# Kernel optimization log

Measured on AMD Instinct MI355X. Metric: run time of the kernel, lower is better.

## Reference

```python
import jax, jax.numpy as jnp
import numpy as np

DIM = 1024
H = 16
DQK = 64   # head_qk_dim = dim*expand_k / num_heads
DV = 64    # head_v_dim
DIN = 4    # dim_inner (fast-weight rows)
CHUNK = 16
BASE_LR = 1e-3
KS = 4     # short conv kernel size
LN_EPS = 1e-5


def short_conv(x, w):
    """Causal depthwise conv1d (kernel KS) + identity residual.
    x: [b, l, c], w: [c, KS] (tap j multiplies x[t - (KS-1) + j])."""
    b, l, c = x.shape
    xp = jnp.pad(x, ((0, 0), (KS - 1, 0), (0, 0)))
    y = x  # residual: y = conv(x) + x
    for j in range(KS):
        y = y + xp[:, j:j + l, :] * w[None, None, :, j]
    return y


def setup_inputs() -> dict:
    key = jax.random.key(0)
    ks = jax.random.split(key, 16)
    b, l = 4, 2048
    key_dim, value_dim = H * DQK, H * DV
    inp = {
        "hidden_states": jax.random.normal(ks[0], (b, l, DIM), jnp.float32),
        "Wq": jax.random.normal(ks[1], (key_dim, DIM), jnp.float32) / np.sqrt(DIM),
        "Wk": jax.random.normal(ks[2], (key_dim, DIM), jnp.float32) / np.sqrt(DIM),
        "Wv": jax.random.normal(ks[3], (value_dim, DIM), jnp.float32) / np.sqrt(DIM),
        "Wlr": jax.random.normal(ks[4], (2 * H, DIM), jnp.float32) / np.sqrt(DIM),
        "Wo": jax.random.normal(ks[5], (DIM, value_dim), jnp.float32) / np.sqrt(value_dim),
        "Wg": jax.random.normal(ks[6], (DIM, value_dim), jnp.float32) / np.sqrt(value_dim),
        "conv_q": jax.random.normal(ks[7], (key_dim, KS), jnp.float32) / np.sqrt(KS),
        "conv_k": jax.random.normal(ks[8], (key_dim, KS), jnp.float32) / np.sqrt(KS),
        "conv_v": jax.random.normal(ks[9], (value_dim, KS), jnp.float32) / np.sqrt(KS),
        "W_in_init": jax.random.normal(ks[10], (1, DIN, H, DQK), jnp.float32) / np.sqrt(DQK),
        "W_out_init": jax.random.normal(ks[11], (1, DIN, H, DV), jnp.float32) / np.sqrt(DIN),
        "ln_gamma": jnp.ones((DV,), jnp.float32),
        "ln_beta": jnp.zeros((DV,), jnp.float32),
    }
    return inp


def reference(hidden_states, Wq, Wk, Wv, Wlr, Wo, Wg,
              conv_q, conv_k, conv_v, W_in_init, W_out_init, ln_gamma, ln_beta):
    b, l, _ = hidden_states.shape
    scale = 1.0 / np.sqrt(DQK)

    q = short_conv(hidden_states @ Wq.T, conv_q).reshape(b, l, H, DQK)
    k = short_conv(hidden_states @ Wk.T, conv_k).reshape(b, l, H, DQK)
    v = short_conv(hidden_states @ Wv.T, conv_v).reshape(b, l, H, DV)

    lr = jax.nn.softplus(hidden_states @ Wlr.T + BASE_LR).reshape(b, l, H, 2)

    nC = l // CHUNK
    # [nC, b, CHUNK, H, d] for scan over chunks
    qc = q.reshape(b, nC, CHUNK, H, DQK).transpose(1, 0, 2, 3, 4)
    kc = k.reshape(b, nC, CHUNK, H, DQK).transpose(1, 0, 2, 3, 4)
    vc = v.reshape(b, nC, CHUNK, H, DV).transpose(1, 0, 2, 3, 4)
    lrc = lr.reshape(b, nC, CHUNK, H, 2).transpose(1, 0, 2, 3, 4)

    W_in0 = jnp.broadcast_to(W_in_init, (b, DIN, H, DQK))
    W_out0 = jnp.broadcast_to(W_out_init, (b, DIN, H, DV))

    # causal mask: query t (abs pos DIN+t) sees keys j <= DIN+t
    mask = jnp.arange(DIN + CHUNK)[None, :] <= (jnp.arange(CHUNK)[:, None] + DIN)

    def step(carry, xs):
        W_in, W_out = carry
        qch, kch, vch, lrch = xs  # [b, CHUNK, H, d]
        Kf = jnp.concatenate([W_in, kch], axis=1)   # [b, DIN+CHUNK, H, DQK]
        Vf = jnp.concatenate([W_out, vch], axis=1)  # [b, DIN+CHUNK, H, DV]
        s = jnp.einsum('bthd,bshd->bhts', qch, Kf) * scale
        s = jnp.where(mask[None, None], s, -jnp.inf)
        o = jnp.einsum('bhts,bshd->bthd', jax.nn.softmax(s, axis=-1), Vf)

        # fast_kk update rule (non-causal attention, queries = W_in rows)
        g1 = jnp.einsum('bnhd,bchd->bhnc', W_in, kch) * scale
        Grad_out = -jnp.einsum('bhnc,bchd->bnhd', jax.nn.softmax(g1, -1), vch)
        g2 = jnp.einsum('bnhd,bchd->bhnc', W_in, kch * 0.5) * scale
        Grad_in = -jnp.einsum('bhnc,bchd->bnhd', jax.nn.softmax(g2, -1), kch)

        lr_mean = jnp.mean(lrch, axis=1, keepdims=True)  # [b,1,H,2]
        W_in_new = W_in - lr_mean[..., 0:1] * Grad_in
        W_out_new = W_out - lr_mean[..., 1:2] * Grad_out
        return (W_in_new, W_out_new), o

    _, os = jax.lax.scan(step, (W_in0, W_out0), (qc, kc, vc, lrc))
    o = os.transpose(1, 0, 2, 3, 4).reshape(b, l, H, DV)

    # LayerNorm over head_v_dim
    mu = o.mean(-1, keepdims=True)
    var = o.var(-1, keepdims=True)
    o = (o - mu) / jnp.sqrt(var + LN_EPS) * ln_gamma + ln_beta
    o = o.reshape(b, l, H * DV)

    gate = hidden_states @ Wg.T
    return (o * gate) @ Wo.T
```

## Files before the change

### kernel.cpp

```cpp
#include <hip/hip_runtime.h>
#include <hip/hip_bf16.h>
#include <math.h>

#define BATCH 4
#define SEQ   2048
#define DIM   1024
#define NH    16
#define DQK   64
#define DV    64
#define DIN   4
#define CHUNK 16
#define NC    128
#define KS    4
#define TOK   (BATCH*SEQ)
#define SCALE 0.125f
#define BASE_LR 1e-3f
#define LN_EPS 1e-5f
#define K3    3072

typedef float f32x4 __attribute__((ext_vector_type(4)));
typedef short s16x8 __attribute__((ext_vector_type(8)));

__device__ __forceinline__ unsigned short f2bf(float f) {
    unsigned u = __float_as_uint(f);
    u += 0x7fffu + ((u >> 16) & 1u);
    return (unsigned short)(u >> 16);
}
__device__ __forceinline__ float bf2f(unsigned short h) {
    return __uint_as_float(((unsigned)h) << 16);
}

__device__ __forceinline__ void gload_lds16(const void* g, void* l) {
    __builtin_amdgcn_global_load_lds(
        (const __attribute__((address_space(1))) void*)g,
        (__attribute__((address_space(3))) void*)l, 16, 0, 0);
}

__global__ __launch_bounds__(256) void split_bf16_kernel(
    const float* __restrict__ X, unsigned short* __restrict__ Y,
    int rows, int wmode)
{
    const int idx = blockIdx.x * 256 + threadIdx.x;
    if (idx >= rows * (DIM / 4)) return;
    const int r  = idx >> 8;
    const int c4 = (idx & 255) << 2;

    float4 x = *(const float4*)(X + (size_t)r * DIM + c4);
    ushort4 hv, lv;
    hv.x = f2bf(x.x); lv.x = f2bf(x.x - bf2f(hv.x));
    hv.y = f2bf(x.y); lv.y = f2bf(x.y - bf2f(hv.y));
    hv.z = f2bf(x.z); lv.z = f2bf(x.z - bf2f(hv.z));
    hv.w = f2bf(x.w); lv.w = f2bf(x.w - bf2f(hv.w));

    const size_t rb = (size_t)r * K3;
    *(ushort4*)(Y + rb + c4)        = hv;
    *(ushort4*)(Y + rb + 1024 + c4) = wmode ? lv : hv;
    *(ushort4*)(Y + rb + 2048 + c4) = wmode ? hv : lv;
}

__global__ __launch_bounds__(256) void gemm_mfma_qkvg(
    const unsigned short* __restrict__ A, const unsigned short* __restrict__ B,
    float* __restrict__ Cq, float* __restrict__ Ck,
    float* __restrict__ Cv, float* __restrict__ Cg)
{
    __shared__ __align__(16) unsigned short sA[128 * 64];
    __shared__ __align__(16) unsigned short sB[128 * 64];

    const int tid  = threadIdx.x;
    const int lane = tid & 63;
    const int wav  = tid >> 6;

    const int nbx = gridDim.x;
    const int nwg = nbx * gridDim.y;
    int flat = blockIdx.x + blockIdx.y * nbx;
    const int per = nwg >> 3;
    flat = (flat & 7) * per + (flat >> 3);
    const int m0 = (flat / nbx) * 128;
    const int n0 = (flat % nbx) * 128;

    const int wm = (wav >> 1) * 64;
    const int wn = (wav & 1) * 64;

    f32x4 acc[4][4] = {};

    const int fbase = wav * 64 + lane;
    const int lrow  = lane & 15;
    const int g     = lane >> 4;

    for (int kt = 0; kt < K3; kt += 64) {
        __syncthreads();
#pragma unroll
        for (int i = 0; i < 4; ++i) {
            const int f  = fbase + i * 256;
            const int r  = f >> 3;
            const int c  = (f & 7) ^ (r & 7);
            const size_t go = (size_t)r * K3 + kt + c * 8;
            char* lb = (char*)sA + (wav * 64 + i * 256) * 16;
            gload_lds16(A + (size_t)m0 * K3 + go, lb);
        }
#pragma unroll
        for (int i = 0; i < 4; ++i) {
            const int f  = fbase + i * 256;
            const int r  = f >> 3;
            const int c  = (f & 7) ^ (r & 7);
            const size_t go = (size_t)r * K3 + kt + c * 8;
            char* lb = (char*)sB + (wav * 64 + i * 256) * 16;
            gload_lds16(B + (size_t)n0 * K3 + go, lb);
        }
        __syncthreads();

#pragma unroll
        for (int ks = 0; ks < 2; ++ks) {
            const int cbase = ks * 4 + g;
            s16x8 af[4], bfr[4];
#pragma unroll
            for (int mi = 0; mi < 4; ++mi) {
                const int r  = wm + mi * 16 + lrow;
                const int cs = cbase ^ (r & 7);
                af[mi] = *(const s16x8*)((const char*)sA + r * 128 + cs * 16);
            }
#pragma unroll
            for (int ni = 0; ni < 4; ++ni) {
                const int r  = wn + ni * 16 + lrow;
                const int cs = cbase ^ (r & 7);
                bfr[ni] = *(const s16x8*)((const char*)sB + r * 128 + cs * 16);
            }
#pragma unroll
            for (int mi = 0; mi < 4; ++mi)
#pragma unroll
                for (int ni = 0; ni < 4; ++ni)
                    acc[mi][ni] = __builtin_amdgcn_mfma_f32_16x16x32_bf16(
                        af[mi], bfr[ni], acc[mi][ni], 0, 0, 0);
        }
    }

    const int nblk = n0 >> 10;
    float* __restrict__ Co = (nblk == 0) ? Cq : (nblk == 1) ? Ck
                           : (nblk == 2) ? Cv : Cg;
    const int nc0 = (n0 & 1023) + wn;
    const int lcol = lane & 15;
    const int lq   = lane >> 4;
#pragma unroll
    for (int mi = 0; mi < 4; ++mi)
#pragma unroll
        for (int ni = 0; ni < 4; ++ni)
#pragma unroll
            for (int r = 0; r < 4; ++r) {
                const int m = m0 + wm + mi * 16 + lq * 4 + r;
                const int n = nc0 + ni * 16 + lcol;
                Co[(size_t)m * DIM + n] = acc[mi][ni][r];
            }
}

__global__ __launch_bounds__(256) void gemm_mfma_bt(
    const unsigned short* __restrict__ A, const unsigned short* __restrict__ B,
    float* __restrict__ C, int M, int N)
{
    __shared__ __align__(16) unsigned short sA[128 * 64];
    __shared__ __align__(16) unsigned short sB[128 * 64];

    const int tid  = threadIdx.x;
    const int lane = tid & 63;
    const int wav  = tid >> 6;

    const int nbx = gridDim.x;
    const int nwg = nbx * gridDim.y;
    int flat = blockIdx.x + blockIdx.y * nbx;
    const int per = nwg >> 3;
    flat = (flat & 7) * per + (flat >> 3);
    const int m0 = (flat / nbx) * 128;
    const int n0 = (flat % nbx) * 128;

    const int wm = (wav >> 1) * 64;
    const int wn = (wav & 1) * 64;

    f32x4 acc[4][4] = {};

    const int fbase = wav * 64 + lane;
    const int lrow  = lane & 15;
    const int g     = lane >> 4;

    for (int kt = 0; kt < K3; kt += 64) {
        __syncthreads();
#pragma unroll
        for (int i = 0; i < 4; ++i) {
            const int f  = fbase + i * 256;
            const int r  = f >> 3;
            const int c  = (f & 7) ^ (r & 7);
            const size_t go = (size_t)r * K3 + kt + c * 8;
            char* lb = (char*)sA + (wav * 64 + i * 256) * 16;
            gload_lds16(A + (size_t)m0 * K3 + go, lb);
        }
#pragma unroll
        for (int i = 0; i < 4; ++i) {
            const int f  = fbase + i * 256;
            const int r  = f >> 3;
            const int c  = (f & 7) ^ (r & 7);
            const size_t go = (size_t)r * K3 + kt + c * 8;
            char* lb = (char*)sB + (wav * 64 + i * 256) * 16;
            gload_lds16(B + (size_t)n0 * K3 + go, lb);
        }
        __syncthreads();

#pragma unroll
        for (int ks = 0; ks < 2; ++ks) {
            const int cbase = ks * 4 + g;
            s16x8 af[4], bfr[4];
#pragma unroll
            for (int mi = 0; mi < 4; ++mi) {
                const int r  = wm + mi * 16 + lrow;
                const int cs = cbase ^ (r & 7);
                af[mi] = *(const s16x8*)((const char*)sA + r * 128 + cs * 16);
            }
#pragma unroll
            for (int ni = 0; ni < 4; ++ni) {
                const int r  = wn + ni * 16 + lrow;
                const int cs = cbase ^ (r & 7);
                bfr[ni] = *(const s16x8*)((const char*)sB + r * 128 + cs * 16);
            }
#pragma unroll
            for (int mi = 0; mi < 4; ++mi)
#pragma unroll
                for (int ni = 0; ni < 4; ++ni)
                    acc[mi][ni] = __builtin_amdgcn_mfma_f32_16x16x32_bf16(
                        af[mi], bfr[ni], acc[mi][ni], 0, 0, 0);
        }
    }

    const int lcol = lane & 15;
    const int lq   = lane >> 4;
#pragma unroll
    for (int mi = 0; mi < 4; ++mi)
#pragma unroll
        for (int ni = 0; ni < 4; ++ni)
#pragma unroll
            for (int r = 0; r < 4; ++r) {
                const int m = m0 + wm + mi * 16 + lq * 4 + r;
                const int n = n0 + wn + ni * 16 + lcol;
                C[(size_t)m * N + n] = acc[mi][ni][r];
            }
}

#define GBM 128
#define GBN 128
#define GBK 8

__global__ __launch_bounds__(256) void gemm_nt_f32(
    const float* __restrict__ A, const float* __restrict__ B,
    float* __restrict__ C, int M, int N, int K)
{
    __shared__ float As[GBK][GBM + 4];
    __shared__ float Bs[GBK][GBN + 4];

    const int tid = threadIdx.x;
    const int m0 = blockIdx.y * GBM;
    const int n0 = blockIdx.x * GBN;
    const int la_m = tid >> 1;
    const int la_k = (tid & 1) << 2;
    const int tm = tid >> 4;
    const int tn = tid & 15;

    float acc[8][8] = {};

    const float* Arow = A + (size_t)(m0 + la_m) * K + la_k;
    const float* Brow = B + (size_t)(n0 + la_m) * K + la_k;
    const bool bvalid = (n0 + la_m) < N;

    for (int k0 = 0; k0 < K; k0 += GBK) {
        float4 av = *(const float4*)(Arow + k0);
        float4 bv = make_float4(0.f, 0.f, 0.f, 0.f);
        if (bvalid) bv = *(const float4*)(Brow + k0);

        __syncthreads();
        As[la_k + 0][la_m] = av.x; As[la_k + 1][la_m] = av.y;
        As[la_k + 2][la_m] = av.z; As[la_k + 3][la_m] = av.w;
        Bs[la_k + 0][la_m] = bv.x; Bs[la_k + 1][la_m] = bv.y;
        Bs[la_k + 2][la_m] = bv.z; Bs[la_k + 3][la_m] = bv.w;
        __syncthreads();

#pragma unroll
        for (int k = 0; k < GBK; ++k) {
            float4 a0 = *(const float4*)&As[k][tm * 8];
            float4 a1 = *(const float4*)&As[k][tm * 8 + 4];
            float4 b0 = *(const float4*)&Bs[k][tn * 8];
            float4 b1 = *(const float4*)&Bs[k][tn * 8 + 4];
            float a[8] = {a0.x, a0.y, a0.z, a0.w, a1.x, a1.y, a1.z, a1.w};
            float b[8] = {b0.x, b0.y, b0.z, b0.w, b1.x, b1.y, b1.z, b1.w};
#pragma unroll
            for (int i = 0; i < 8; ++i)
#pragma unroll
                for (int j = 0; j < 8; ++j)
                    acc[i][j] += a[i] * b[j];
        }
    }

#pragma unroll
    for (int i = 0; i < 8; ++i) {
        const int m = m0 + tm * 8 + i;
#pragma unroll
        for (int j = 0; j < 8; ++j) {
            const int n = n0 + tn * 8 + j;
            if (n < N) C[(size_t)m * N + n] = acc[i][j];
        }
    }
}

__global__ __launch_bounds__(256) void conv_res_kernel(
    const float* __restrict__ x, const float* __restrict__ w,
    float* __restrict__ y)
{
    const int tid = blockIdx.x * blockDim.x + threadIdx.x;
    if (tid >= TOK * 256) return;
    const int c4  = (tid & 255) << 2;
    const int row = tid >> 8;
    const int t   = row & (SEQ - 1);

    const float* xp = x + (size_t)row * DIM + c4;
    float4 acc = *(const float4*)xp;
    float4 w0 = *(const float4*)(w + (c4 + 0) * 4);
    float4 w1 = *(const float4*)(w + (c4 + 1) * 4);
    float4 w2 = *(const float4*)(w + (c4 + 2) * 4);
    float4 w3 = *(const float4*)(w + (c4 + 3) * 4);

#pragma unroll
    for (int j = 0; j < 4; ++j) {
        const int tt = t - 3 + j;
        if (tt >= 0) {
            float4 xv = *(const float4*)(xp + (j - 3) * DIM);
            acc.x += xv.x * ((&w0.x)[j]);
            acc.y += xv.y * ((&w1.x)[j]);
            acc.z += xv.z * ((&w2.x)[j]);
            acc.w += xv.w * ((&w3.x)[j]);
        }
    }
    *(float4*)(y + (size_t)row * DIM + c4) = acc;
}

__global__ __launch_bounds__(256) void lrmean_kernel(
    const float* __restrict__ lrpre, float* __restrict__ lrm)
{
    const int idx = blockIdx.x * blockDim.x + threadIdx.x;
    if (idx >= BATCH * NC * NH * 2) return;
    const int j = idx & 1;
    const int h = (idx >> 1) & 15;
    const int c = (idx >> 5) & 127;
    const int b = idx >> 12;

    float s = 0.f;
#pragma unroll
    for (int i = 0; i < CHUNK; ++i) {
        float x = lrpre[((size_t)b * SEQ + c * CHUNK + i) * 32 + h * 2 + j] + BASE_LR;
        s += fmaxf(x, 0.f) + log1pf(expf(-fabsf(x)));
    }
    lrm[idx] = s * (1.f / CHUNK);
}

__global__ __launch_bounds__(128) void state_scan_kernel(
    const float* __restrict__ kconv, const float* __restrict__ vconv,
    const float* __restrict__ lrm,
    const float* __restrict__ win_init, const float* __restrict__ wout_init,
    float* __restrict__ wst_in, float* __restrict__ wst_out)
{
    const int bh  = blockIdx.x;
    const int b   = bh >> 4, h = bh & 15;
    const int tid = threadIdx.x;
    const int wv  = tid >> 6;
    const int d   = tid & 63;

    __shared__ __align__(16) float sW[DIN][68];
    __shared__ __align__(16) float sK[CHUNK][68];
    __shared__ __align__(16) float sP1[2][DIN][16];
    __shared__ __align__(16) float sP2[2][DIN][16];
    __shared__ float sLR[NC * 2];

    const float* __restrict__ xin  = wv ? vconv     : kconv;
    const float* __restrict__ wini = wv ? wout_init : win_init;
    float*       __restrict__ wst  = wv ? wst_out   : wst_in;

    float W[DIN];
#pragma unroll
    for (int n = 0; n < DIN; ++n) W[n] = wini[(n * NH + h) * 64 + d];

    sLR[tid * 2 + 0] = lrm[(((size_t)b * NC + tid) * NH + h) * 2 + 0];
    sLR[tid * 2 + 1] = lrm[(((size_t)b * NC + tid) * NH + h) * 2 + 1];

    const int gn = d >> 4;
    const int gc = d & 15;

    float xa[CHUNK], xb[CHUNK];
    const size_t base00 = (size_t)b * SEQ * DIM + h * 64 + d;
#pragma unroll
    for (int i = 0; i < CHUNK; ++i) xa[i] = xin[base00 + (size_t)i * DIM];
    asm volatile("s_waitcnt lgkmcnt(0)" ::: "memory");

#define SCAN_STEP(c, XA, XB)                                                   \
    {                                                                          \
        const int pb = (c) & 1;                                                \
        if ((c) + 1 < NC) {                                                    \
            const size_t basen = base00 + (size_t)(((c) + 1) * CHUNK) * DIM;   \
            _Pragma("unroll")                                                  \
            for (int i = 0; i < CHUNK; ++i)                                    \
                XB[i] = xin[basen + (size_t)i * DIM];                          \
        }                                                                      \
        const size_t wofs = (((size_t)bh * NC + (c)) * DIN) * 64 + d;          \
        _Pragma("unroll")                                                      \
        for (int n = 0; n < DIN; ++n) wst[wofs + n * 64] = W[n];               \
        if (wv == 0) {                                                         \
            _Pragma("unroll")                                                  \
            for (int i = 0; i < CHUNK; ++i) sK[i][d] = XA[i];                  \
            _Pragma("unroll")                                                  \
            for (int n = 0; n < DIN; ++n) sW[n][d] = W[n];                     \
            asm volatile("s_waitcnt lgkmcnt(0)" ::: "memory");                 \
            float p0 = 0.f, p1 = 0.f, p2 = 0.f, p3 = 0.f;                      \
            _Pragma("unroll")                                                  \
            for (int q = 0; q < 4; ++q) {                                      \
                const int o = q * 16;                                          \
                float4 w0 = *(const float4*)&sW[gn][o + 0];                    \
                float4 k0 = *(const float4*)&sK[gc][o + 0];                    \
                float4 w1 = *(const float4*)&sW[gn][o + 4];                    \
                float4 k1 = *(const float4*)&sK[gc][o + 4];                    \
                float4 w2 = *(const float4*)&sW[gn][o + 8];                    \
                float4 k2 = *(const float4*)&sK[gc][o + 8];                    \
                float4 w3 = *(const float4*)&sW[gn][o + 12];                   \
                float4 k3 = *(const float4*)&sK[gc][o + 12];                   \
                p0 += w0.x*k0.x; p0 += w0.y*k0.y; p0 += w0.z*k0.z; p0 += w0.w*k0.w; \
                p1 += w1.x*k1.x; p1 += w1.y*k1.y; p1 += w1.z*k1.z; p1 += w1.w*k1.w; \
                p2 += w2.x*k2.x; p2 += w2.y*k2.y; p2 += w2.z*k2.z; p2 += w2.w*k2.w; \
                p3 += w3.x*k3.x; p3 += w3.y*k3.y; p3 += w3.z*k3.z; p3 += w3.w*k3.w; \
            }                                                                  \
            const float g1 = ((p0 + p1) + (p2 + p3)) * SCALE;                  \
            float m = g1;                                                      \
            _Pragma("unroll")                                                  \
            for (int mk = 8; mk >= 1; mk >>= 1)                                \
                m = fmaxf(m, __shfl_xor(m, mk, 16));                           \
            const float e1 = expf(g1 - m);                                     \
            const float rr = sqrtf(e1);                 \
            float s1 = e1, s2 = rr;                                            \
            _Pragma("unroll")                                                  \
            for (int mk = 8; mk >= 1; mk >>= 1) {                              \
                s1 += __shfl_xor(s1, mk, 16);                                  \
                s2 += __shfl_xor(s2, mk, 16);                                  \
            }                                                                  \
            sP1[pb][gn][gc] = e1 / s1;                                         \
            sP2[pb][gn][gc] = rr / s2;                                         \
            asm volatile("s_waitcnt lgkmcnt(0)" ::: "memory");                 \
        }                                                                      \
        __builtin_amdgcn_s_barrier();                                          \
        const float lr = sLR[(c) * 2 + wv];                                    \
        const float (*P)[16] = wv ? sP1[pb] : sP2[pb];                         \
        _Pragma("unroll")                                                      \
        for (int n = 0; n < DIN; ++n) {                                        \
            float4 q0 = *(const float4*)&P[n][0];                              \
            float4 q1 = *(const float4*)&P[n][4];                              \
            float4 q2 = *(const float4*)&P[n][8];                              \
            float4 q3 = *(const float4*)&P[n][12];                             \
            float t0 = q0.x*XA[0];  t0 += q0.y*XA[1];                          \
            t0 += q0.z*XA[2];       t0 += q0.w*XA[3];                          \
            float t1 = q1.x*XA[4];  t1 += q1.y*XA[5];                          \
            t1 += q1.z*XA[6];       t1 += q1.w*XA[7];                          \
            float t2 = q2.x*XA[8];  t2 += q2.y*XA[9];                          \
            t2 += q2.z*XA[10];      t2 += q2.w*XA[11];                         \
            float t3 = q3.x*XA[12]; t3 += q3.y*XA[13];                         \
            t3 += q3.z*XA[14];      t3 += q3.w*XA[15];                         \
            W[n] += lr * ((t0 + t1) + (t2 + t3));                              \
        }                                                                      \
    }

    for (int c = 0; c < NC; c += 2) {
        SCAN_STEP(c,     xa, xb);
        SCAN_STEP(c + 1, xb, xa);
    }
#undef SCAN_STEP
}

__global__ __launch_bounds__(64) void attn_kernel(
    const float* __restrict__ qconv, const float* __restrict__ kconv,
    const float* __restrict__ vconv,
    const float* __restrict__ wst_in, const float* __restrict__ wst_out,
    const float* __restrict__ gate,
    const float* __restrict__ gamma, const float* __restrict__ beta,
    float* __restrict__ og)
{
    const int blk = blockIdx.x;
    const int c  = blk & (NC - 1);
    const int bh = blk >> 7;
    const int h = bh & 15, b = bh >> 4;
    const int d = threadIdx.x;

    __shared__ float sQ[CHUNK][65];
    __shared__ float sKf[DIN + CHUNK][65];
    __shared__ float sS[CHUNK][21];
    __shared__ float sO[CHUNK][65];
    __shared__ float sMu[CHUNK], sRs[CHUNK];

    float vf[DIN + CHUNK];

    const size_t wofs = (size_t)blk * (DIN * 64) + d;
#pragma unroll
    for (int n = 0; n < DIN; ++n) {
        sKf[n][d] = wst_in [wofs + n * 64];
        vf[n]     = wst_out[wofs + n * 64];
    }
    const size_t base = ((size_t)b * SEQ + c * CHUNK) * DIM + h * 64 + d;
#pragma unroll
    for (int i = 0; i < CHUNK; ++i) {
        sQ[i][d]        = qconv[base + (size_t)i * DIM];
        sKf[DIN + i][d] = kconv[base + (size_t)i * DIM];
        vf[DIN + i]     = vconv[base + (size_t)i * DIM];
    }
    __syncthreads();

#pragma unroll
    for (int r = 0; r < 5; ++r) {
        const int p = d + 64 * r;
        const int t = p / 20, j = p % 20;
        float dot = 0.f;
#pragma unroll
        for (int dd = 0; dd < 64; ++dd) dot += sQ[t][dd] * sKf[j][dd];
        float s = dot * SCALE;
        if (j >= DIN && (j - DIN) > t) s = -3.0e38f;
        sS[t][j] = s;
    }
    __syncthreads();

    if (d < CHUNK) {
        float m = -3.0e38f;
#pragma unroll
        for (int j = 0; j < DIN + CHUNK; ++j) m = fmaxf(m, sS[d][j]);
        float e[DIN + CHUNK];
        float sum = 0.f;
#pragma unroll
        for (int j = 0; j < DIN + CHUNK; ++j) { e[j] = expf(sS[d][j] - m); sum += e[j]; }
        const float inv = 1.f / sum;
#pragma unroll
        for (int j = 0; j < DIN + CHUNK; ++j) sS[d][j] = e[j] * inv;
    }
    __syncthreads();

#pragma unroll
    for (int t = 0; t < CHUNK; ++t) {
        float o = 0.f;
#pragma unroll
        for (int j = 0; j < DIN + CHUNK; ++j) o += sS[t][j] * vf[j];
        sO[t][d] = o;
    }
    __syncthreads();

    if (d < CHUNK) {
        float su = 0.f, sq = 0.f;
#pragma unroll
        for (int dd = 0; dd < 64; ++dd) { float x = sO[d][dd]; su += x; sq += x * x; }
        float mu = su * (1.f / 64.f);
        float var = sq * (1.f / 64.f) - mu * mu;
        sMu[d] = mu;
        sRs[d] = rsqrtf(var + LN_EPS);
    }
    __syncthreads();

    const float gm = gamma[d], bt = beta[d];
#pragma unroll
    for (int t = 0; t < CHUNK; ++t) {
        float val = (sO[t][d] - sMu[t]) * sRs[t] * gm + bt;
        float gval = gate[base + (size_t)t * DIM];
        og[base + (size_t)t * DIM] = val * gval;
    }
}

extern "C" void kernel_launch(void* const* d_in, const int* in_sizes, int n_in,
                              void* d_out, int out_size, void* d_ws, size_t ws_size,
                              hipStream_t stream)
{
    const float* hid   = (const float*)d_in[0];
    const float* Wq    = (const float*)d_in[1];
    const float* Wk    = (const float*)d_in[2];
    const float* Wv    = (const float*)d_in[3];
    const float* Wlr   = (const float*)d_in[4];
    const float* Wo    = (const float*)d_in[5];
    const float* Wg    = (const float*)d_in[6];
    const float* cq    = (const float*)d_in[7];
    const float* ck    = (const float*)d_in[8];
    const float* cv    = (const float*)d_in[9];
    const float* wini  = (const float*)d_in[10];
    const float* wouti = (const float*)d_in[11];
    const float* lng   = (const float*)d_in[12];
    const float* lnb   = (const float*)d_in[13];
    float* out = (float*)d_out;

    float* ws = (float*)d_ws;
    const size_t DSZ = (size_t)TOK * DIM;
    float* qraw  = ws;
    float* kraw  = qraw + DSZ;
    float* vraw  = kraw + DSZ;
    float* gatb  = vraw + DSZ;
    float* lrpre = gatb + DSZ;
    float* lrm   = lrpre + (size_t)TOK * 32;
    float* wsti  = lrm   + BATCH * NC * NH * 2;
    float* wsto  = wsti  + (size_t)BATCH * NH * NC * DIN * 64;
    unsigned short* Abuf = (unsigned short*)(wsto + (size_t)BATCH * NH * NC * DIN * 64);
    unsigned short* Bbuf = Abuf + (size_t)TOK * K3;
    float* spar = (float*)Bbuf;

    float* qv = spar;
    float* kv = qraw;
    float* vv = kraw;

    const dim3 blk256(256);
    const dim3 fused_grid(32, 64);
    const dim3 out_grid(8, 64);
    const dim3 gemm_grid_lr(1, TOK / GBM);
    const int conv_blocks = (TOK * 256 + 255) / 256;

    split_bf16_kernel<<<TOK, blk256, 0, stream>>>(hid, Abuf, TOK, 0);
    split_bf16_kernel<<<1024, blk256, 0, stream>>>(Wq, Bbuf,                       1024, 1);
    split_bf16_kernel<<<1024, blk256, 0, stream>>>(Wk, Bbuf + (size_t)1024 * K3,   1024, 1);
    split_bf16_kernel<<<1024, blk256, 0, stream>>>(Wv, Bbuf + (size_t)2048 * K3,   1024, 1);
    split_bf16_kernel<<<1024, blk256, 0, stream>>>(Wg, Bbuf + (size_t)3072 * K3,   1024, 1);

    gemm_mfma_qkvg<<<fused_grid, blk256, 0, stream>>>(Abuf, Bbuf, qraw, kraw, vraw, gatb);

    conv_res_kernel<<<conv_blocks, blk256, 0, stream>>>(qraw, cq, spar);
    conv_res_kernel<<<conv_blocks, blk256, 0, stream>>>(kraw, ck, qraw);
    conv_res_kernel<<<conv_blocks, blk256, 0, stream>>>(vraw, cv, kraw);

    gemm_nt_f32<<<gemm_grid_lr, blk256, 0, stream>>>(hid, Wlr, lrpre, TOK, 32, DIM);
    lrmean_kernel<<<(BATCH * NC * NH * 2 + 255) / 256, blk256, 0, stream>>>(lrpre, lrm);

    state_scan_kernel<<<BATCH * NH, 128, 0, stream>>>(kv, vv, lrm, wini, wouti, wsti, wsto);
    attn_kernel<<<BATCH * NH * NC, 64, 0, stream>>>(qv, kv, vv, wsti, wsto,
                                                    gatb, lng, lnb, qv);

    split_bf16_kernel<<<TOK, blk256, 0, stream>>>(qv, Abuf, TOK, 0);
    split_bf16_kernel<<<1024, blk256, 0, stream>>>(Wo, Bbuf, 1024, 1);
    gemm_mfma_bt<<<out_grid, blk256, 0, stream>>>(Abuf, Bbuf, out, TOK, DIM);
}
```

Measured before the change: 917.8 us.

## Use 256x256 double-buffered QKVG GEMM and move Wlr projection to split-K MFMA

```diff
diff --git a/kernel.cpp b/kernel.cpp
--- a/kernel.cpp
+++ b/kernel.cpp
@@ -58,10 +58,137 @@
     *(ushort4*)(Y + rb + 2048 + c4) = wmode ? hv : lv;
 }
 
-__global__ __launch_bounds__(256) void gemm_mfma_qkvg(
+__global__ __launch_bounds__(512, 1) void gemm_mfma_qkvg(
     const unsigned short* __restrict__ A, const unsigned short* __restrict__ B,
     float* __restrict__ Cq, float* __restrict__ Ck,
     float* __restrict__ Cv, float* __restrict__ Cg)
+{
+    __shared__ __align__(16) unsigned short sA[2][256 * 64];
+    __shared__ __align__(16) unsigned short sB[2][256 * 64];
+
+    const int tid  = threadIdx.x;
+    const int lane = tid & 63;
+    const int wid  = tid >> 6;
+
+    const int nbx = gridDim.x;
+    const int nwg = nbx * gridDim.y;
+    int flat = blockIdx.x + blockIdx.y * nbx;
+    const int per = nwg >> 3;
+    flat = (flat & 7) * per + (flat >> 3);
+    const int m0 = (flat / nbx) * 256;
+    const int n0 = (flat % nbx) * 256;
+
+    const int wm = (wid >> 2) * 128;
+    const int wn = (wid & 3) * 64;
+
+    f32x4 acc[8][4] = {};
+
+    const int lrow = lane & 15;
+    const int g    = lane >> 4;
+
+#define SL_A(db, ktile, i)                                                     \
+    do {                                                                       \
+        const int f_ = tid + (i) * 512;                                        \
+        const int r_ = f_ >> 3;                                                \
+        const int c_ = (f_ & 7) ^ (r_ & 7);                                    \
+        gload_lds16(A + (size_t)(m0 + r_) * K3 + (ktile) * 64 + c_ * 8,        \
+                    (char*)sA[db] + (wid * 64 + (i) * 512) * 16);              \
+    } while (0)
+#define SL_B(db, ktile, i)                                                     \
+    do {                                                                       \
+        const int f_ = tid + (i) * 512;                                        \
+        const int r_ = f_ >> 3;                                                \
+        const int c_ = (f_ & 7) ^ (r_ & 7);                                    \
+        gload_lds16(B + (size_t)(n0 + r_) * K3 + (ktile) * 64 + c_ * 8,        \
+                    (char*)sB[db] + (wid * 64 + (i) * 512) * 16);              \
+    } while (0)
+
+#define PHASE(db, ks, mh, SCODE)                                               \
+    do {                                                                       \
+        SCODE;                                                                 \
+        const char* pA_ = (const char*)sA[db];                                 \
+        const char* pB_ = (const char*)sB[db];                                 \
+        s16x8 af[4], bfr[4];                                                   \
+        _Pragma("unroll")                                                      \
+        for (int j = 0; j < 4; ++j) {                                          \
+            const int r_  = wm + ((mh) * 4 + j) * 16 + lrow;                   \
+            const int cs_ = ((ks) * 4 + g) ^ (r_ & 7);                         \
+            af[j] = *(const s16x8*)(pA_ + r_ * 128 + cs_ * 16);                \
+        }                                                                      \
+        _Pragma("unroll")                                                      \
+        for (int ni = 0; ni < 4; ++ni) {                                       \
+            const int r_  = wn + ni * 16 + lrow;                               \
+            const int cs_ = ((ks) * 4 + g) ^ (r_ & 7);                         \
+            bfr[ni] = *(const s16x8*)(pB_ + r_ * 128 + cs_ * 16);              \
+        }                                                                      \
+        asm volatile("" ::: "memory");                                         \
+        __builtin_amdgcn_s_barrier();                                          \
+        asm volatile("s_waitcnt lgkmcnt(0)" ::: "memory");                     \
+        __builtin_amdgcn_s_setprio(1);                                         \
+        _Pragma("unroll")                                                      \
+        for (int j = 0; j < 4; ++j)                                            \
+            _Pragma("unroll")                                                  \
+            for (int ni = 0; ni < 4; ++ni)                                     \
+                acc[(mh) * 4 + j][ni] = __builtin_amdgcn_mfma_f32_16x16x32_bf16( \
+                    af[j], bfr[ni], acc[(mh) * 4 + j][ni], 0, 0, 0);           \
+        __builtin_amdgcn_s_setprio(0);                                         \
+        asm volatile("" ::: "memory");                                         \
+        __builtin_amdgcn_s_barrier();                                          \
+        asm volatile("" ::: "memory");                                         \
+    } while (0)
+
+    SL_A(0, 0, 0); SL_A(0, 0, 1); SL_A(0, 0, 2); SL_A(0, 0, 3);
+    SL_B(0, 0, 0); SL_B(0, 0, 1); SL_B(0, 0, 2); SL_B(0, 0, 3);
+
+    const int NT = K3 / 64;
+    for (int i = 0; i < NT / 2; ++i) {
+        const int t1 = 2 * i + 1;
+        const int t2 = 2 * i + 2;
+        const bool more = (t2 < NT);
+
+        asm volatile("s_waitcnt vmcnt(0)" ::: "memory");
+        asm volatile("" ::: "memory");
+        __builtin_amdgcn_s_barrier();
+
+        PHASE(0, 0, 0, { SL_A(1, t1, 0); SL_A(1, t1, 1); SL_A(1, t1, 2); });
+        PHASE(0, 0, 1, { SL_A(1, t1, 3); SL_B(1, t1, 0); SL_B(1, t1, 1); });
+        PHASE(0, 1, 0, { SL_B(1, t1, 2); SL_B(1, t1, 3); });
+        PHASE(0, 1, 1, { });
+
+        asm volatile("s_waitcnt vmcnt(0)" ::: "memory");
+        asm volatile("" ::: "memory");
+        __builtin_amdgcn_s_barrier();
+
+        PHASE(1, 0, 0, { if (more) { SL_A(0, t2, 0); SL_A(0, t2, 1); SL_A(0, t2, 2); } });
+        PHASE(1, 0, 1, { if (more) { SL_A(0, t2, 3); SL_B(0, t2, 0); SL_B(0, t2, 1); } });
+        PHASE(1, 1, 0, { if (more) { SL_B(0, t2, 2); SL_B(0, t2, 3); } });
+        PHASE(1, 1, 1, { });
+    }
+#undef PHASE
+#undef SL_A
+#undef SL_B
+
+    const int nblk = n0 >> 10;
+    float* __restrict__ Co = (nblk == 0) ? Cq : (nblk == 1) ? Ck
+                           : (nblk == 2) ? Cv : Cg;
+    const int nc0 = (n0 & 1023) + wn;
+    const int lcol = lane & 15;
+    const int lq   = lane >> 4;
+#pragma unroll
+    for (int mi = 0; mi < 8; ++mi)
+#pragma unroll
+        for (int ni = 0; ni < 4; ++ni)
+#pragma unroll
+            for (int r = 0; r < 4; ++r) {
+                const int m = m0 + wm + mi * 16 + lq * 4 + r;
+                const int n = nc0 + ni * 16 + lcol;
+                Co[(size_t)m * DIM + n] = acc[mi][ni][r];
+            }
+}
+
+__global__ __launch_bounds__(256) void gemm_mfma_bt(
+    const unsigned short* __restrict__ A, const unsigned short* __restrict__ B,
+    float* __restrict__ C, int M, int N)
 {
     __shared__ __align__(16) unsigned short sA[128 * 64];
     __shared__ __align__(16) unsigned short sB[128 * 64];
@@ -134,10 +261,6 @@
         }
     }
 
-    const int nblk = n0 >> 10;
-    float* __restrict__ Co = (nblk == 0) ? Cq : (nblk == 1) ? Ck
-                           : (nblk == 2) ? Cv : Cg;
-    const int nc0 = (n0 & 1023) + wn;
     const int lcol = lane & 15;
     const int lq   = lane >> 4;
 #pragma unroll
@@ -147,14 +270,14 @@
 #pragma unroll
             for (int r = 0; r < 4; ++r) {
                 const int m = m0 + wm + mi * 16 + lq * 4 + r;
-                const int n = nc0 + ni * 16 + lcol;
-                Co[(size_t)m * DIM + n] = acc[mi][ni][r];
+                const int n = n0 + wn + ni * 16 + lcol;
+                C[(size_t)m * N + n] = acc[mi][ni][r];
             }
 }
 
-__global__ __launch_bounds__(256) void gemm_mfma_bt(
-    const unsigned short* __restrict__ A, const unsigned short* __restrict__ B,
-    float* __restrict__ C, int M, int N)
+__global__ __launch_bounds__(256) void gemm_mfma_lr(
+    const unsigned short* __restrict__ A, const unsigned short* __restrict__ Bl,
+    float* __restrict__ lrp)
 {
     __shared__ __align__(16) unsigned short sA[128 * 64];
     __shared__ __align__(16) unsigned short sB[128 * 64];
@@ -162,14 +285,8 @@
     const int tid  = threadIdx.x;
     const int lane = tid & 63;
     const int wav  = tid >> 6;
-
-    const int nbx = gridDim.x;
-    const int nwg = nbx * gridDim.y;
-    int flat = blockIdx.x + blockIdx.y * nbx;
-    const int per = nwg >> 3;
-    flat = (flat & 7) * per + (flat >> 3);
-    const int m0 = (flat / nbx) * 128;
-    const int n0 = (flat % nbx) * 128;
+    const int kb   = blockIdx.x;
+    const int m0   = blockIdx.y * 128;
 
     const int wm = (wav >> 1) * 64;
     const int wn = (wav & 1) * 64;
@@ -180,25 +297,24 @@
     const int lrow  = lane & 15;
     const int g     = lane >> 4;
 
-    for (int kt = 0; kt < K3; kt += 64) {
+    const int k0 = kb * (K3 / 4);
+    for (int kt = k0; kt < k0 + K3 / 4; kt += 64) {
         __syncthreads();
 #pragma unroll
         for (int i = 0; i < 4; ++i) {
             const int f  = fbase + i * 256;
             const int r  = f >> 3;
             const int c  = (f & 7) ^ (r & 7);
-            const size_t go = (size_t)r * K3 + kt + c * 8;
-            char* lb = (char*)sA + (wav * 64 + i * 256) * 16;
-            gload_lds16(A + (size_t)m0 * K3 + go, lb);
+            gload_lds16(A + (size_t)(m0 + r) * K3 + kt + c * 8,
+                        (char*)sA + (wav * 64 + i * 256) * 16);
         }
 #pragma unroll
         for (int i = 0; i < 4; ++i) {
             const int f  = fbase + i * 256;
             const int r  = f >> 3;
             const int c  = (f & 7) ^ (r & 7);
-            const size_t go = (size_t)r * K3 + kt + c * 8;
-            char* lb = (char*)sB + (wav * 64 + i * 256) * 16;
-            gload_lds16(B + (size_t)n0 * K3 + go, lb);
+            gload_lds16(Bl + (size_t)r * K3 + kt + c * 8,
+                        (char*)sB + (wav * 64 + i * 256) * 16);
         }
         __syncthreads();
 
@@ -227,82 +343,20 @@
         }
     }
 
+    if (wn != 0) return;
     const int lcol = lane & 15;
     const int lq   = lane >> 4;
+    float* dst = lrp + (size_t)kb * TOK * 32;
 #pragma unroll
     for (int mi = 0; mi < 4; ++mi)
 #pragma unroll
-        for (int ni = 0; ni < 4; ++ni)
+        for (int ni = 0; ni < 2; ++ni)
 #pragma unroll
             for (int r = 0; r < 4; ++r) {
                 const int m = m0 + wm + mi * 16 + lq * 4 + r;
-                const int n = n0 + wn + ni * 16 + lcol;
-                C[(size_t)m * N + n] = acc[mi][ni][r];
+                const int n = ni * 16 + lcol;
+                dst[(size_t)m * 32 + n] = acc[mi][ni][r];
             }
-}
-
-#define GBM 128
-#define GBN 128
-#define GBK 8
-
-__global__ __launch_bounds__(256) void gemm_nt_f32(
-    const float* __restrict__ A, const float* __restrict__ B,
-    float* __restrict__ C, int M, int N, int K)
-{
-    __shared__ float As[GBK][GBM + 4];
-    __shared__ float Bs[GBK][GBN + 4];
-
-    const int tid = threadIdx.x;
-    const int m0 = blockIdx.y * GBM;
-    const int n0 = blockIdx.x * GBN;
-    const int la_m = tid >> 1;
-    const int la_k = (tid & 1) << 2;
-    const int tm = tid >> 4;
-    const int tn = tid & 15;
-
-    float acc[8][8] = {};
-
-    const float* Arow = A + (size_t)(m0 + la_m) * K + la_k;
-    const float* Brow = B + (size_t)(n0 + la_m) * K + la_k;
-    const bool bvalid = (n0 + la_m) < N;
-
-    for (int k0 = 0; k0 < K; k0 += GBK) {
-        float4 av = *(const float4*)(Arow + k0);
-        float4 bv = make_float4(0.f, 0.f, 0.f, 0.f);
-        if (bvalid) bv = *(const float4*)(Brow + k0);
-
-        __syncthreads();
-        As[la_k + 0][la_m] = av.x; As[la_k + 1][la_m] = av.y;
-        As[la_k + 2][la_m] = av.z; As[la_k + 3][la_m] = av.w;
-        Bs[la_k + 0][la_m] = bv.x; Bs[la_k + 1][la_m] = bv.y;
-        Bs[la_k + 2][la_m] = bv.z; Bs[la_k + 3][la_m] = bv.w;
-        __syncthreads();
-
-#pragma unroll
-        for (int k = 0; k < GBK; ++k) {
-            float4 a0 = *(const float4*)&As[k][tm * 8];
-            float4 a1 = *(const float4*)&As[k][tm * 8 + 4];
-            float4 b0 = *(const float4*)&Bs[k][tn * 8];
-            float4 b1 = *(const float4*)&Bs[k][tn * 8 + 4];
-            float a[8] = {a0.x, a0.y, a0.z, a0.w, a1.x, a1.y, a1.z, a1.w};
-            float b[8] = {b0.x, b0.y, b0.z, b0.w, b1.x, b1.y, b1.z, b1.w};
-#pragma unroll
-            for (int i = 0; i < 8; ++i)
-#pragma unroll
-                for (int j = 0; j < 8; ++j)
-                    acc[i][j] += a[i] * b[j];
-        }
-    }
-
-#pragma unroll
-    for (int i = 0; i < 8; ++i) {
-        const int m = m0 + tm * 8 + i;
-#pragma unroll
-        for (int j = 0; j < 8; ++j) {
-            const int n = n0 + tn * 8 + j;
-            if (n < N) C[(size_t)m * N + n] = acc[i][j];
-        }
-    }
 }
 
 __global__ __launch_bounds__(256) void conv_res_kernel(
@@ -337,7 +391,7 @@
 }
 
 __global__ __launch_bounds__(256) void lrmean_kernel(
-    const float* __restrict__ lrpre, float* __restrict__ lrm)
+    const float* __restrict__ lrp, float* __restrict__ lrm)
 {
     const int idx = blockIdx.x * blockDim.x + threadIdx.x;
     if (idx >= BATCH * NC * NH * 2) return;
@@ -346,10 +400,13 @@
     const int c = (idx >> 5) & 127;
     const int b = idx >> 12;
 
+    const size_t T32 = (size_t)TOK * 32;
     float s = 0.f;
 #pragma unroll
     for (int i = 0; i < CHUNK; ++i) {
-        float x = lrpre[((size_t)b * SEQ + c * CHUNK + i) * 32 + h * 2 + j] + BASE_LR;
+        const size_t e = ((size_t)b * SEQ + c * CHUNK + i) * 32 + h * 2 + j;
+        float x = ((lrp[e] + lrp[T32 + e]) + (lrp[2 * T32 + e] + lrp[3 * T32 + e]))
+                  + BASE_LR;
         s += fmaxf(x, 0.f) + log1pf(expf(-fabsf(x)));
     }
     lrm[idx] = s * (1.f / CHUNK);
@@ -592,22 +649,23 @@
     float* kraw  = qraw + DSZ;
     float* vraw  = kraw + DSZ;
     float* gatb  = vraw + DSZ;
-    float* lrpre = gatb + DSZ;
-    float* lrm   = lrpre + (size_t)TOK * 32;
-    float* wsti  = lrm   + BATCH * NC * NH * 2;
-    float* wsto  = wsti  + (size_t)BATCH * NH * NC * DIN * 64;
+    float* lrp   = gatb + DSZ;
+    float* lrm   = lrp  + (size_t)TOK * 128;
+    float* wsti  = lrm  + BATCH * NC * NH * 2;
+    float* wsto  = wsti + (size_t)BATCH * NH * NC * DIN * 64;
     unsigned short* Abuf = (unsigned short*)(wsto + (size_t)BATCH * NH * NC * DIN * 64);
     unsigned short* Bbuf = Abuf + (size_t)TOK * K3;
     float* spar = (float*)Bbuf;
+    unsigned short* WlrB = (unsigned short*)(spar + DSZ);
 
     float* qv = spar;
     float* kv = qraw;
     float* vv = kraw;
 
     const dim3 blk256(256);
-    const dim3 fused_grid(32, 64);
+    const dim3 fused_grid(16, 32);
+    const dim3 lr_grid(4, 64);
     const dim3 out_grid(8, 64);
-    const dim3 gemm_grid_lr(1, TOK / GBM);
     const int conv_blocks = (TOK * 256 + 255) / 256;
 
     split_bf16_kernel<<<TOK, blk256, 0, stream>>>(hid, Abuf, TOK, 0);
@@ -615,15 +673,17 @@
     split_bf16_kernel<<<1024, blk256, 0, stream>>>(Wk, Bbuf + (size_t)1024 * K3,   1024, 1);
     split_bf16_kernel<<<1024, blk256, 0, stream>>>(Wv, Bbuf + (size_t)2048 * K3,   1024, 1);
     split_bf16_kernel<<<1024, blk256, 0, stream>>>(Wg, Bbuf + (size_t)3072 * K3,   1024, 1);
-
-    gemm_mfma_qkvg<<<fused_grid, blk256, 0, stream>>>(Abuf, Bbuf, qraw, kraw, vraw, gatb);
+    split_bf16_kernel<<<32,   blk256, 0, stream>>>(Wlr, WlrB,                        32, 1);
+
+    gemm_mfma_qkvg<<<fused_grid, 512, 0, stream>>>(Abuf, Bbuf, qraw, kraw, vraw, gatb);
+
+    gemm_mfma_lr<<<lr_grid, blk256, 0, stream>>>(Abuf, WlrB, lrp);
 
     conv_res_kernel<<<conv_blocks, blk256, 0, stream>>>(qraw, cq, spar);
     conv_res_kernel<<<conv_blocks, blk256, 0, stream>>>(kraw, ck, qraw);
     conv_res_kernel<<<conv_blocks, blk256, 0, stream>>>(vraw, cv, kraw);
 
-    gemm_nt_f32<<<gemm_grid_lr, blk256, 0, stream>>>(hid, Wlr, lrpre, TOK, 32, DIM);
-    lrmean_kernel<<<(BATCH * NC * NH * 2 + 255) / 256, blk256, 0, stream>>>(lrpre, lrm);
+    lrmean_kernel<<<(BATCH * NC * NH * 2 + 255) / 256, blk256, 0, stream>>>(lrp, lrm);
 
     state_scan_kernel<<<BATCH * NH, 128, 0, stream>>>(kv, vv, lrm, wini, wouti, wsti, wsto);
     attn_kernel<<<BATCH * NH * NC, 64, 0, stream>>>(qv, kv, vv, wsti, wsto,
```

Result: faster. 795.8 us (-13.3%).
